# Kernel tuning notes

Measured on AMD Instinct MI355X. Metric: run time of the kernel, lower is better.

The kernel has to match this reference:

```python
import jax, jax.numpy as jnp
import numpy as np

K = 128   # per-head dim == input dim
H = 8     # heads
B = 2
T = 2048


def setup_inputs() -> dict:
    key = jax.random.key(0)
    ks = jax.random.split(key, 6)
    s_in = 1.0 / np.sqrt(K)
    s_out = 1.0 / np.sqrt(K * H)
    return {
        "x": jax.random.normal(ks[0], (B, T, K), dtype=jnp.float32),
        # Linear weights stored as (in, out); torch Linear init ~ U(-1/sqrt(in), 1/sqrt(in))
        "Wq": jax.random.uniform(ks[1], (K, K * H), jnp.float32, -s_in, s_in),
        "Wk": jax.random.uniform(ks[2], (K, K * H), jnp.float32, -s_in, s_in),
        "Wv": jax.random.uniform(ks[3], (K, K * H), jnp.float32, -s_in, s_in),
        "Wo": jax.random.uniform(ks[4], (K * H, K), jnp.float32, -s_out, s_out),
        "bo": jax.random.uniform(ks[5], (K,), jnp.float32, -s_out, s_out),
    }


def reference(x, Wq, Wk, Wv, Wo, bo):
    b, t, k = x.shape
    h = H
    scale = k ** 0.25
    # projections -> [b, t, h, k]
    q = (x @ Wq).reshape(b, t, h, k) / scale
    ke = (x @ Wk).reshape(b, t, h, k) / scale
    v = (x @ Wv).reshape(b, t, h, k)
    # scores: [b, h, t, t]
    scores = jnp.einsum('bihk,bjhk->bhij', q, ke)
    # causal mask: positions j > i get -inf (diagonal kept)
    causal = jnp.tril(jnp.ones((t, t), dtype=bool))
    scores = jnp.where(causal[None, None], scores, -jnp.inf)
    p = jax.nn.softmax(scores, axis=-1)
    out = jnp.einsum('bhij,bjhk->bihk', p, v).reshape(b, t, h * k)
    return out @ Wo + bo
```

## Files before the change

### kernel.cpp

```cpp
#include <hip/hip_runtime.h>

typedef __bf16 bf16;
typedef __bf16 bf16x4 __attribute__((ext_vector_type(4)));
typedef __bf16 bf16x8 __attribute__((ext_vector_type(8)));
typedef float f32x4 __attribute__((ext_vector_type(4)));
typedef float f32x16 __attribute__((ext_vector_type(16)));
typedef int i32x4 __attribute__((ext_vector_type(4)));

#define MFMA16(a, b, c) __builtin_amdgcn_mfma_f32_16x16x32_bf16((a), (b), (c), 0, 0, 0)
#define MFMA32(a, b, c) __builtin_amdgcn_mfma_f32_32x32x16_bf16((a), (b), (c), 0, 0, 0)

__device__ __forceinline__ int swz16(int r, int c) { return (c ^ (r & 15)); }

__device__ __forceinline__ int cvt_pk_bf16(float lo, float hi) {
  int r;
  asm("v_cvt_pk_bf16_f32 %0, %1, %2" : "=v"(r) : "v"(lo), "v"(hi));
  return r;
}

__global__ __launch_bounds__(256) void trW_kernel(
    const float* __restrict__ Wq, const float* __restrict__ Wk,
    const float* __restrict__ Wv, const float* __restrict__ Wo,
    bf16* __restrict__ outbase) {
  __shared__ bf16 tile[32][33];
  const int z = blockIdx.z;
  const float* ib = (z == 0) ? Wq : (z == 1) ? Wk : (z == 2) ? Wv : Wo;
  bf16* ob = outbase + (size_t)z * 131072;
  const int R = (z < 3) ? 128 : 1024;
  const int C = (z < 3) ? 1024 : 128;
  int r0 = (z < 3) ? blockIdx.y * 32 : blockIdx.x * 32;
  int c0 = (z < 3) ? blockIdx.x * 32 : blockIdx.y * 32;
  int tx = threadIdx.x & 31, ty = threadIdx.x >> 5;
#pragma unroll
  for (int i = 0; i < 4; ++i) {
    int r = ty + i * 8;
    tile[r][tx] = (bf16)ib[(size_t)(r0 + r) * C + (c0 + tx)];
  }
  __syncthreads();
#pragma unroll
  for (int i = 0; i < 4; ++i) {
    int r = ty + i * 8;
    ob[(size_t)(c0 + r) * R + (r0 + tx)] = tile[tx][r];
  }
}

__global__ __launch_bounds__(256) void proj_gemm(
    const float* __restrict__ x, const bf16* __restrict__ Wqt,
    const bf16* __restrict__ Wkt, const bf16* __restrict__ Wvt,
    bf16* __restrict__ Qf, bf16* __restrict__ Kf, bf16* __restrict__ Vf) {
  __shared__ __align__(16) bf16 As[128 * 128];
  __shared__ __align__(16) bf16 Bs[128 * 128];
  const int mt = blockIdx.x;
  const int nt = blockIdx.y;
  const int matid = nt >> 3, h = nt & 7;
  const bf16* W = (matid == 0) ? Wqt : (matid == 1) ? Wkt : Wvt;
  const int tid = threadIdx.x;
  const bf16* sb = W + (size_t)h * 128 * 128;
#pragma unroll
  for (int i = 0; i < 8; ++i) {
    int c = tid + i * 256;
    int r = c >> 4, cc = c & 15;
    const f32x4* p = (const f32x4*)(x + (size_t)(mt * 128 + r) * 128 + cc * 8);
    f32x4 a = p[0], b = p[1];
    bf16x8 o;
#pragma unroll
    for (int j = 0; j < 4; ++j) { o[j] = (bf16)a[j]; o[4 + j] = (bf16)b[j]; }
    *(bf16x8*)&As[r * 128 + swz16(r, cc) * 8] = o;
  }
#pragma unroll
  for (int i = 0; i < 8; ++i) {
    int c = tid + i * 256;
    int r = c >> 4, cc = c & 15;
    *(bf16x8*)&Bs[r * 128 + swz16(r, cc) * 8] = *(const bf16x8*)(sb + (size_t)r * 128 + cc * 8);
  }
  __syncthreads();
  const int wave = tid >> 6, lane = tid & 63;
  const int wr = (wave >> 1) * 64, wc = (wave & 1) * 64;
  const int lr = lane & 15, lkb = lane >> 4;
  const f32x4 FZ = {0.f, 0.f, 0.f, 0.f};
  f32x4 acc[4][4];
#pragma unroll
  for (int mf = 0; mf < 4; ++mf)
#pragma unroll
    for (int nf = 0; nf < 4; ++nf) acc[mf][nf] = FZ;
  const bool qk = (matid < 2);
#pragma unroll
  for (int ks = 0; ks < 4; ++ks) {
    bf16x8 a[4], b[4];
#pragma unroll
    for (int mf = 0; mf < 4; ++mf) {
      int r = wr + mf * 16 + lr;
      a[mf] = *(const bf16x8*)&As[r * 128 + swz16(r, ks * 4 + lkb) * 8];
    }
#pragma unroll
    for (int nf = 0; nf < 4; ++nf) {
      int r = wc + nf * 16 + lr;
      b[nf] = *(const bf16x8*)&Bs[r * 128 + swz16(r, ks * 4 + lkb) * 8];
    }
    if (qk) {
#pragma unroll
      for (int mf = 0; mf < 4; ++mf)
#pragma unroll
        for (int nf = 0; nf < 4; ++nf) acc[mf][nf] = MFMA16(b[nf], a[mf], acc[mf][nf]);
    } else {
#pragma unroll
      for (int mf = 0; mf < 4; ++mf)
#pragma unroll
        for (int nf = 0; nf < 4; ++nf) acc[mf][nf] = MFMA16(a[mf], b[nf], acc[mf][nf]);
    }
  }
  const int rb = lkb * 4;
  if (qk) {
    bf16* Out = (matid == 0) ? Qf : Kf;
#pragma unroll
    for (int mf = 0; mf < 4; ++mf)
#pragma unroll
      for (int nf = 0; nf < 4; ++nf) {
        int m = mt * 128 + wr + mf * 16 + lr;
        int d0 = wc + nf * 16 + rb;
        int bb = m >> 11, t = m & 2047;
        bf16x4 vv;
#pragma unroll
        for (int r = 0; r < 4; ++r) vv[r] = (bf16)acc[mf][nf][r];
        size_t e = (size_t)(bb * 8 + h) * 262144
                 + (size_t)(((t >> 5) * 8 + (d0 >> 4)) * 512 + ((d0 >> 3) & 1) * 256
                            + (t & 31) * 8 + (d0 & 7));
        *(bf16x4*)(Out + e) = vv;
      }
  } else {
#pragma unroll
    for (int mf = 0; mf < 4; ++mf)
#pragma unroll
      for (int nf = 0; nf < 4; ++nf) {
        int d = wc + nf * 16 + lr;
        int m0 = mt * 128 + wr + mf * 16 + rb;
        int bb = m0 >> 11, t0 = m0 & 2047;
        bf16x4 vv;
#pragma unroll
        for (int r = 0; r < 4; ++r) vv[r] = (bf16)acc[mf][nf][r];
        size_t e = (size_t)(bb * 8 + h) * 262144
                 + (size_t)((d >> 5) * 65536 + (t0 >> 4) * 512 + ((t0 >> 3) & 1) * 256
                            + (d & 31) * 8 + (t0 & 7));
        *(bf16x4*)(Vf + e) = vv;
      }
  }
}

__global__ __launch_bounds__(128) void attn_kernel(
    bf16* __restrict__ Qf, const bf16* __restrict__ Kf, const bf16* __restrict__ Vf) {
  __shared__ float Om[128 * 32];
  __shared__ float Lm[32];
  __shared__ float Ll[32];
  const int bid = blockIdx.x;
  const int bh = (bid & 7) | (((bid >> 3) & 1) << 3);
  const int j = bid >> 4;
  const int v = j & 15, m4 = j >> 4;
  const int qt = (m4 == 0) ? v : (m4 == 1) ? 31 - v : (m4 == 2) ? 32 + v : 63 - v;
  const int nT = (qt >> 1) + 1;
  const int h0 = (nT + 1) >> 1, h1 = nT - h0;
  const int tid = threadIdx.x;
  const int g = tid >> 6, lane = tid & 63;
  const int lq = lane & 31, hi = lane >> 5;
  const int q0 = qt * 32;
  const int hg = g ? h1 : h0;
  const int tb = g ? h0 : 0;
  const bf16* Qh = Qf + (size_t)bh * 262144;
  const bf16* Kh = Kf + (size_t)bh * 262144;
  const bf16* Vh = Vf + (size_t)bh * 262144;
  const float SCL = 0.12751744f;
  const int lo = hi * 256 + lq * 8;

  bf16x8 qf[8];
#pragma unroll
  for (int ks = 0; ks < 8; ++ks)
    qf[ks] = *(const bf16x8*)(Qh + qt * 4096 + ks * 512 + lo);

  float mrun = -__builtin_inff(), lrun = 0.f;
  f32x16 O[4];
#pragma unroll
  for (int dt = 0; dt < 4; ++dt)
#pragma unroll
    for (int r = 0; r < 16; ++r) O[dt][r] = 0.f;

  for (int it = 0; it < hg; ++it) {
    const int kvt = tb + it;
    const int kv0 = kvt * 64;
    const bf16* kbase = Kh + kvt * 8192 + lo;
    bf16x8 ka[8], kb[8];
#pragma unroll
    for (int i = 0; i < 8; ++i) ka[i] = *(const bf16x8*)(kbase + i * 512);
#pragma unroll
    for (int i = 0; i < 8; ++i) kb[i] = *(const bf16x8*)(kbase + 4096 + i * 512);
    f32x16 p0, p1;
#pragma unroll
    for (int r = 0; r < 16; ++r) { p0[r] = 0.f; p1[r] = 0.f; }
#pragma unroll
    for (int ks = 0; ks < 8; ++ks) p0 = MFMA32(ka[ks], qf[ks], p0);
#pragma unroll
    for (int ks = 0; ks < 8; ++ks) p1 = MFMA32(kb[ks], qf[ks], p1);
    if (kvt == (qt >> 1)) {
      const int qg = q0 + lq;
#pragma unroll
      for (int r = 0; r < 16; ++r) {
        int kvr = kv0 + (r & 3) + 8 * (r >> 2) + 4 * hi;
        if (kvr > qg) p0[r] = -__builtin_inff();
        if (kvr + 32 > qg) p1[r] = -__builtin_inff();
      }
    }
    float pm = -__builtin_inff();
#pragma unroll
    for (int r = 0; r < 16; ++r) pm = fmaxf(pm, fmaxf(p0[r], p1[r]));
    pm = fmaxf(pm, __shfl_xor(pm, 32, 64));
    float pmS = pm * SCL;
    if (!__all(pmS <= mrun + 8.f)) {
      float mnew = fmaxf(mrun, pmS);
      float alpha = exp2f(mrun - mnew);
      mrun = mnew;
      lrun *= alpha;
#pragma unroll
      for (int dt = 0; dt < 4; ++dt)
#pragma unroll
        for (int r = 0; r < 16; ++r) O[dt][r] *= alpha;
    }
    float ps = 0.f;
#pragma unroll
    for (int r = 0; r < 16; ++r) {
      float a = exp2f(__builtin_fmaf(p0[r], SCL, -mrun));
      float b = exp2f(__builtin_fmaf(p1[r], SCL, -mrun));
      p0[r] = a; p1[r] = b;
      ps += a + b;
    }
    ps += __shfl_xor(ps, 32, 64);
    lrun += ps;
    int w[16];
#pragma unroll
    for (int i = 0; i < 8; ++i) w[i] = cvt_pk_bf16(p0[2 * i], p0[2 * i + 1]);
#pragma unroll
    for (int i = 0; i < 8; ++i) w[8 + i] = cvt_pk_bf16(p1[2 * i], p1[2 * i + 1]);
    bf16x8 pa[4];
#pragma unroll
    for (int t4 = 0; t4 < 4; ++t4) {
      int b0 = t4 * 4;
      int e0 = __shfl_xor(w[b0 + 0], 32, 64);
      int e1 = __shfl_xor(w[b0 + 1], 32, 64);
      int e2 = __shfl_xor(w[b0 + 2], 32, 64);
      int e3 = __shfl_xor(w[b0 + 3], 32, 64);
      i32x4 f;
      f[0] = hi ? e2 : w[b0 + 0];
      f[1] = hi ? e3 : w[b0 + 1];
      f[2] = hi ? w[b0 + 2] : e0;
      f[3] = hi ? w[b0 + 3] : e1;
      pa[t4] = __builtin_bit_cast(bf16x8, f);
    }
    const bf16* vbase = Vh + (kvt * 4) * 512 + lo;
#pragma unroll
    for (int dt = 0; dt < 4; ++dt) {
      bf16x8 va0 = *(const bf16x8*)(vbase + dt * 65536 + 0 * 512);
      bf16x8 va1 = *(const bf16x8*)(vbase + dt * 65536 + 1 * 512);
      bf16x8 va2 = *(const bf16x8*)(vbase + dt * 65536 + 2 * 512);
      bf16x8 va3 = *(const bf16x8*)(vbase + dt * 65536 + 3 * 512);
      O[dt] = MFMA32(va0, pa[0], O[dt]);
      O[dt] = MFMA32(va1, pa[1], O[dt]);
      O[dt] = MFMA32(va2, pa[2], O[dt]);
      O[dt] = MFMA32(va3, pa[3], O[dt]);
    }
  }

  if (g == 1) {
#pragma unroll
    for (int dt = 0; dt < 4; ++dt)
#pragma unroll
      for (int r = 0; r < 16; ++r)
        Om[(dt * 32 + (r & 3) + 8 * (r >> 2) + 4 * hi) * 32 + lq] = O[dt][r];
    if (!hi) { Lm[lq] = mrun; Ll[lq] = lrun; }
  }
  __syncthreads();
  if (g == 0) {
    float m1 = Lm[lq], l1 = Ll[lq];
    float mF = fmaxf(mrun, m1);
    float a0 = exp2f(mrun - mF), a1 = exp2f(m1 - mF);
    float inv = 1.f / (lrun * a0 + l1 * a1);
    bf16* qw = Qf + (size_t)bh * 262144 + qt * 4096 + lq * 8 + 4 * hi;
#pragma unroll
    for (int dt = 0; dt < 4; ++dt) {
#pragma unroll
      for (int rq = 0; rq < 4; ++rq) {
        bf16x4 vv;
#pragma unroll
        for (int jj = 0; jj < 4; ++jj) {
          int r = rq * 4 + jj;
          int d = dt * 32 + jj + 8 * rq + 4 * hi;
          float o1 = Om[d * 32 + lq];
          vv[jj] = (bf16)((O[dt][r] * a0 + o1 * a1) * inv);
        }
        *(bf16x4*)(qw + (dt * 2 + (rq >> 1)) * 512 + (rq & 1) * 256) = vv;
      }
    }
  }
}

__global__ __launch_bounds__(256) void outproj_kernel(
    const bf16* __restrict__ AO, const bf16* __restrict__ Wot,
    const float* __restrict__ bo, float* __restrict__ out) {
  __shared__ __align__(16) bf16 As[16 * 128];
  __shared__ __align__(16) bf16 Bs[128 * 128];
  const f32x4 FZ = {0.f, 0.f, 0.f, 0.f};
  const int mt = blockIdx.x;
  const int tid = threadIdx.x, wave = tid >> 6, lane = tid & 63;
  const int lr = lane & 15, lkb = lane >> 4, rb = lkb * 4;
  const int wc = wave * 32;
  f32x4 acc[2];
  acc[0] = FZ; acc[1] = FZ;
  for (int kt = 0; kt < 8; ++kt) {
    __syncthreads();
    {
      int r = tid >> 4, cc = tid & 15;
      int m = mt * 16 + r, bb = m >> 11, t = m & 2047;
      const bf16* src = AO + (size_t)(bb * 8 + kt) * 262144
          + ((t >> 5) * 8 + (cc >> 1)) * 512 + (cc & 1) * 256 + (t & 31) * 8;
      *(bf16x8*)&As[r * 128 + swz16(r, cc) * 8] = *(const bf16x8*)src;
    }
#pragma unroll
    for (int i = 0; i < 8; ++i) {
      int c = tid + i * 256;
      int r = c >> 4, cc = c & 15;
      *(bf16x8*)&Bs[r * 128 + swz16(r, cc) * 8] =
          *(const bf16x8*)(Wot + (size_t)r * 1024 + kt * 128 + cc * 8);
    }
    __syncthreads();
#pragma unroll
    for (int ks = 0; ks < 4; ++ks) {
      bf16x8 a = *(const bf16x8*)&As[lr * 128 + swz16(lr, ks * 4 + lkb) * 8];
#pragma unroll
      for (int nf = 0; nf < 2; ++nf) {
        int r = wc + nf * 16 + lr;
        bf16x8 b = *(const bf16x8*)&Bs[r * 128 + swz16(r, ks * 4 + lkb) * 8];
        acc[nf] = MFMA16(a, b, acc[nf]);
      }
    }
  }
#pragma unroll
  for (int nf = 0; nf < 2; ++nf)
#pragma unroll
    for (int r = 0; r < 4; ++r) {
      int m = mt * 16 + rb + r;
      int n = wc + nf * 16 + lr;
      out[(size_t)m * 128 + n] = acc[nf][r] + bo[n];
    }
}

extern "C" void kernel_launch(void* const* d_in, const int* in_sizes, int n_in,
                              void* d_out, int out_size, void* d_ws, size_t ws_size,
                              hipStream_t stream) {
  (void)in_sizes; (void)n_in; (void)out_size; (void)ws_size;
  const float* x  = (const float*)d_in[0];
  const float* Wq = (const float*)d_in[1];
  const float* Wk = (const float*)d_in[2];
  const float* Wv = (const float*)d_in[3];
  const float* Wo = (const float*)d_in[4];
  const float* bo = (const float*)d_in[5];
  float* out = (float*)d_out;

  bf16* ws  = (bf16*)d_ws;
  bf16* Wqt = ws;
  bf16* Wkt = Wqt + 131072;
  bf16* Wvt = Wkt + 131072;
  bf16* Wot = Wvt + 131072;
  bf16* Qf  = Wot + 131072;
  bf16* Kf  = Qf + 4194304;
  bf16* Vf  = Kf + 4194304;

  trW_kernel<<<dim3(32, 4, 4), 256, 0, stream>>>(Wq, Wk, Wv, Wo, Wqt);
  proj_gemm<<<dim3(32, 24, 1), 256, 0, stream>>>(x, Wqt, Wkt, Wvt, Qf, Kf, Vf);
  attn_kernel<<<dim3(1024, 1, 1), 128, 0, stream>>>(Qf, Kf, Vf);
  outproj_kernel<<<dim3(256, 1, 1), 256, 0, stream>>>(Qf, Wot, bo, out);
}
```

Measured before the change: 146.5 us.

## Split causal KV range across four waves and pair query tiles per block

The attention kernel now runs 256 threads per block, and each block handles two complementary query tiles (pr and 63-pr) in sequence so causal work is balanced across blocks. The KV range of each tile is split across four waves, with the split direction reversed in the second phase, and the partial results are merged through a two-level shared-memory reduction with extra barriers. The change also prefetches V fragments before the softmax, raises wave priority around the MFMA sections, and splits the max and sum reductions into four independent chains for more ILP. The cost is more register pressure from holding V in registers, more LDS use, and more synchronization, in exchange for halving the grid and getting more even per-block work.

```diff
diff --git a/kernel.cpp b/kernel.cpp
--- a/kernel.cpp
+++ b/kernel.cpp
@@ -146,156 +146,199 @@
   }
 }
 
-__global__ __launch_bounds__(128) void attn_kernel(
+__global__ __launch_bounds__(256) void attn_kernel(
     bf16* __restrict__ Qf, const bf16* __restrict__ Kf, const bf16* __restrict__ Vf) {
-  __shared__ float Om[128 * 32];
-  __shared__ float Lm[32];
-  __shared__ float Ll[32];
+  __shared__ float Om0[128 * 32];
+  __shared__ float Om1[128 * 32];
+  __shared__ float L0m[32], L0l[32], L1m[32], L1l[32];
   const int bid = blockIdx.x;
-  const int bh = (bid & 7) | (((bid >> 3) & 1) << 3);
-  const int j = bid >> 4;
-  const int v = j & 15, m4 = j >> 4;
-  const int qt = (m4 == 0) ? v : (m4 == 1) ? 31 - v : (m4 == 2) ? 32 + v : 63 - v;
-  const int nT = (qt >> 1) + 1;
-  const int h0 = (nT + 1) >> 1, h1 = nT - h0;
+  const int bh = bid & 15;
+  const int pr = bid >> 4;
   const int tid = threadIdx.x;
-  const int g = tid >> 6, lane = tid & 63;
+  const int w = tid >> 6, lane = tid & 63;
   const int lq = lane & 31, hi = lane >> 5;
-  const int q0 = qt * 32;
-  const int hg = g ? h1 : h0;
-  const int tb = g ? h0 : 0;
+  const int lo = hi * 256 + lq * 8;
   const bf16* Qh = Qf + (size_t)bh * 262144;
   const bf16* Kh = Kf + (size_t)bh * 262144;
   const bf16* Vh = Vf + (size_t)bh * 262144;
   const float SCL = 0.12751744f;
-  const int lo = hi * 256 + lq * 8;
-
-  bf16x8 qf[8];
-#pragma unroll
-  for (int ks = 0; ks < 8; ++ks)
-    qf[ks] = *(const bf16x8*)(Qh + qt * 4096 + ks * 512 + lo);
-
-  float mrun = -__builtin_inff(), lrun = 0.f;
-  f32x16 O[4];
-#pragma unroll
-  for (int dt = 0; dt < 4; ++dt)
-#pragma unroll
-    for (int r = 0; r < 16; ++r) O[dt][r] = 0.f;
-
-  for (int it = 0; it < hg; ++it) {
-    const int kvt = tb + it;
-    const int kv0 = kvt * 64;
-    const bf16* kbase = Kh + kvt * 8192 + lo;
-    bf16x8 ka[8], kb[8];
-#pragma unroll
-    for (int i = 0; i < 8; ++i) ka[i] = *(const bf16x8*)(kbase + i * 512);
-#pragma unroll
-    for (int i = 0; i < 8; ++i) kb[i] = *(const bf16x8*)(kbase + 4096 + i * 512);
-    f32x16 p0, p1;
-#pragma unroll
-    for (int r = 0; r < 16; ++r) { p0[r] = 0.f; p1[r] = 0.f; }
-#pragma unroll
-    for (int ks = 0; ks < 8; ++ks) p0 = MFMA32(ka[ks], qf[ks], p0);
-#pragma unroll
-    for (int ks = 0; ks < 8; ++ks) p1 = MFMA32(kb[ks], qf[ks], p1);
-    if (kvt == (qt >> 1)) {
-      const int qg = q0 + lq;
-#pragma unroll
-      for (int r = 0; r < 16; ++r) {
-        int kvr = kv0 + (r & 3) + 8 * (r >> 2) + 4 * hi;
-        if (kvr > qg) p0[r] = -__builtin_inff();
-        if (kvr + 32 > qg) p1[r] = -__builtin_inff();
-      }
-    }
-    float pm = -__builtin_inff();
-#pragma unroll
-    for (int r = 0; r < 16; ++r) pm = fmaxf(pm, fmaxf(p0[r], p1[r]));
-    pm = fmaxf(pm, __shfl_xor(pm, 32, 64));
-    float pmS = pm * SCL;
-    if (!__all(pmS <= mrun + 8.f)) {
-      float mnew = fmaxf(mrun, pmS);
-      float alpha = exp2f(mrun - mnew);
-      mrun = mnew;
-      lrun *= alpha;
+
+  for (int ph = 0; ph < 2; ++ph) {
+    const int qt = ph ? (63 - pr) : pr;
+    const int nT = (qt >> 1) + 1;
+    const int base = nT >> 2, rem = nT & 3;
+    const int we = ph ? (3 - w) : w;
+    const int cnt = base + (we < rem ? 1 : 0);
+    const int tb = we * base + (we < rem ? we : rem);
+
+    bf16x8 qf[8];
+#pragma unroll
+    for (int ks = 0; ks < 8; ++ks)
+      qf[ks] = *(const bf16x8*)(Qh + qt * 4096 + ks * 512 + lo);
+
+    float mrun = -__builtin_inff(), lrun = 0.f;
+    f32x16 O[4];
+#pragma unroll
+    for (int dt = 0; dt < 4; ++dt)
+#pragma unroll
+      for (int r = 0; r < 16; ++r) O[dt][r] = 0.f;
+
+    for (int it = 0; it < cnt; ++it) {
+      const int kvt = tb + it;
+      const int kv0 = kvt * 64;
+      const bf16* kbase = Kh + kvt * 8192 + lo;
+      bf16x8 ka[8], kb[8];
+#pragma unroll
+      for (int i = 0; i < 8; ++i) ka[i] = *(const bf16x8*)(kbase + i * 512);
+#pragma unroll
+      for (int i = 0; i < 8; ++i) kb[i] = *(const bf16x8*)(kbase + 4096 + i * 512);
+      f32x16 p0, p1;
+#pragma unroll
+      for (int r = 0; r < 16; ++r) { p0[r] = 0.f; p1[r] = 0.f; }
+      __builtin_amdgcn_s_setprio(1);
+#pragma unroll
+      for (int ks = 0; ks < 8; ++ks) p0 = MFMA32(ka[ks], qf[ks], p0);
+#pragma unroll
+      for (int ks = 0; ks < 8; ++ks) p1 = MFMA32(kb[ks], qf[ks], p1);
+      __builtin_amdgcn_s_setprio(0);
+      const bf16* vbase = Vh + kvt * 2048 + lo;
+      bf16x8 va[16];
+#pragma unroll
+      for (int i = 0; i < 16; ++i)
+        va[i] = *(const bf16x8*)(vbase + (i >> 2) * 65536 + (i & 3) * 512);
+      if (kvt == (qt >> 1)) {
+        const int qg = qt * 32 + lq;
+#pragma unroll
+        for (int r = 0; r < 16; ++r) {
+          int kvr = kv0 + (r & 3) + 8 * (r >> 2) + 4 * hi;
+          if (kvr > qg) p0[r] = -__builtin_inff();
+          if (kvr + 32 > qg) p1[r] = -__builtin_inff();
+        }
+      }
+      float m0 = fmaxf(p0[0], p1[0]);
+      float m1_ = fmaxf(p0[1], p1[1]);
+      float m2 = fmaxf(p0[2], p1[2]);
+      float m3 = fmaxf(p0[3], p1[3]);
+#pragma unroll
+      for (int r = 4; r < 16; r += 4) {
+        m0 = fmaxf(m0, fmaxf(p0[r], p1[r]));
+        m1_ = fmaxf(m1_, fmaxf(p0[r + 1], p1[r + 1]));
+        m2 = fmaxf(m2, fmaxf(p0[r + 2], p1[r + 2]));
+        m3 = fmaxf(m3, fmaxf(p0[r + 3], p1[r + 3]));
+      }
+      float pm = fmaxf(fmaxf(m0, m1_), fmaxf(m2, m3));
+      pm = fmaxf(pm, __shfl_xor(pm, 32, 64));
+      float pmS = pm * SCL;
+      if (!__all(pmS <= mrun + 8.f)) {
+        float mnew = fmaxf(mrun, pmS);
+        float alpha = exp2f(mrun - mnew);
+        mrun = mnew;
+        lrun *= alpha;
+#pragma unroll
+        for (int dt = 0; dt < 4; ++dt)
+#pragma unroll
+          for (int r = 0; r < 16; ++r) O[dt][r] *= alpha;
+      }
+      float s0 = 0.f, s1 = 0.f, s2 = 0.f, s3 = 0.f;
+#pragma unroll
+      for (int r = 0; r < 16; r += 4) {
+        float a0_ = exp2f(__builtin_fmaf(p0[r], SCL, -mrun));
+        float a1_ = exp2f(__builtin_fmaf(p0[r + 1], SCL, -mrun));
+        float a2_ = exp2f(__builtin_fmaf(p0[r + 2], SCL, -mrun));
+        float a3_ = exp2f(__builtin_fmaf(p0[r + 3], SCL, -mrun));
+        float b0_ = exp2f(__builtin_fmaf(p1[r], SCL, -mrun));
+        float b1_ = exp2f(__builtin_fmaf(p1[r + 1], SCL, -mrun));
+        float b2_ = exp2f(__builtin_fmaf(p1[r + 2], SCL, -mrun));
+        float b3_ = exp2f(__builtin_fmaf(p1[r + 3], SCL, -mrun));
+        p0[r] = a0_; p0[r + 1] = a1_; p0[r + 2] = a2_; p0[r + 3] = a3_;
+        p1[r] = b0_; p1[r + 1] = b1_; p1[r + 2] = b2_; p1[r + 3] = b3_;
+        s0 += a0_ + b0_; s1 += a1_ + b1_; s2 += a2_ + b2_; s3 += a3_ + b3_;
+      }
+      float ps = (s0 + s1) + (s2 + s3);
+      ps += __shfl_xor(ps, 32, 64);
+      lrun += ps;
+      int wd[16];
+#pragma unroll
+      for (int i = 0; i < 8; ++i) wd[i] = cvt_pk_bf16(p0[2 * i], p0[2 * i + 1]);
+#pragma unroll
+      for (int i = 0; i < 8; ++i) wd[8 + i] = cvt_pk_bf16(p1[2 * i], p1[2 * i + 1]);
+      bf16x8 pa[4];
+#pragma unroll
+      for (int t4 = 0; t4 < 4; ++t4) {
+        int b0 = t4 * 4;
+        int e0 = __shfl_xor(wd[b0 + 0], 32, 64);
+        int e1 = __shfl_xor(wd[b0 + 1], 32, 64);
+        int e2 = __shfl_xor(wd[b0 + 2], 32, 64);
+        int e3 = __shfl_xor(wd[b0 + 3], 32, 64);
+        i32x4 f;
+        f[0] = hi ? e2 : wd[b0 + 0];
+        f[1] = hi ? e3 : wd[b0 + 1];
+        f[2] = hi ? wd[b0 + 2] : e0;
+        f[3] = hi ? wd[b0 + 3] : e1;
+        pa[t4] = __builtin_bit_cast(bf16x8, f);
+      }
+      __builtin_amdgcn_s_setprio(1);
+#pragma unroll
+      for (int dt = 0; dt < 4; ++dt) {
+        O[dt] = MFMA32(va[dt * 4 + 0], pa[0], O[dt]);
+        O[dt] = MFMA32(va[dt * 4 + 1], pa[1], O[dt]);
+        O[dt] = MFMA32(va[dt * 4 + 2], pa[2], O[dt]);
+        O[dt] = MFMA32(va[dt * 4 + 3], pa[3], O[dt]);
+      }
+      __builtin_amdgcn_s_setprio(0);
+    }
+
+    auto STORE = [&](float* Om, float* Lm, float* Ll) {
 #pragma unroll
       for (int dt = 0; dt < 4; ++dt)
 #pragma unroll
-        for (int r = 0; r < 16; ++r) O[dt][r] *= alpha;
-    }
-    float ps = 0.f;
-#pragma unroll
-    for (int r = 0; r < 16; ++r) {
-      float a = exp2f(__builtin_fmaf(p0[r], SCL, -mrun));
-      float b = exp2f(__builtin_fmaf(p1[r], SCL, -mrun));
-      p0[r] = a; p1[r] = b;
-      ps += a + b;
-    }
-    ps += __shfl_xor(ps, 32, 64);
-    lrun += ps;
-    int w[16];
-#pragma unroll
-    for (int i = 0; i < 8; ++i) w[i] = cvt_pk_bf16(p0[2 * i], p0[2 * i + 1]);
-#pragma unroll
-    for (int i = 0; i < 8; ++i) w[8 + i] = cvt_pk_bf16(p1[2 * i], p1[2 * i + 1]);
-    bf16x8 pa[4];
-#pragma unroll
-    for (int t4 = 0; t4 < 4; ++t4) {
-      int b0 = t4 * 4;
-      int e0 = __shfl_xor(w[b0 + 0], 32, 64);
-      int e1 = __shfl_xor(w[b0 + 1], 32, 64);
-      int e2 = __shfl_xor(w[b0 + 2], 32, 64);
-      int e3 = __shfl_xor(w[b0 + 3], 32, 64);
-      i32x4 f;
-      f[0] = hi ? e2 : w[b0 + 0];
-      f[1] = hi ? e3 : w[b0 + 1];
-      f[2] = hi ? w[b0 + 2] : e0;
-      f[3] = hi ? w[b0 + 3] : e1;
-      pa[t4] = __builtin_bit_cast(bf16x8, f);
-    }
-    const bf16* vbase = Vh + (kvt * 4) * 512 + lo;
-#pragma unroll
-    for (int dt = 0; dt < 4; ++dt) {
-      bf16x8 va0 = *(const bf16x8*)(vbase + dt * 65536 + 0 * 512);
-      bf16x8 va1 = *(const bf16x8*)(vbase + dt * 65536 + 1 * 512);
-      bf16x8 va2 = *(const bf16x8*)(vbase + dt * 65536 + 2 * 512);
-      bf16x8 va3 = *(const bf16x8*)(vbase + dt * 65536 + 3 * 512);
-      O[dt] = MFMA32(va0, pa[0], O[dt]);
-      O[dt] = MFMA32(va1, pa[1], O[dt]);
-      O[dt] = MFMA32(va2, pa[2], O[dt]);
-      O[dt] = MFMA32(va3, pa[3], O[dt]);
-    }
-  }
-
-  if (g == 1) {
-#pragma unroll
-    for (int dt = 0; dt < 4; ++dt)
-#pragma unroll
-      for (int r = 0; r < 16; ++r)
-        Om[(dt * 32 + (r & 3) + 8 * (r >> 2) + 4 * hi) * 32 + lq] = O[dt][r];
-    if (!hi) { Lm[lq] = mrun; Ll[lq] = lrun; }
-  }
-  __syncthreads();
-  if (g == 0) {
-    float m1 = Lm[lq], l1 = Ll[lq];
-    float mF = fmaxf(mrun, m1);
-    float a0 = exp2f(mrun - mF), a1 = exp2f(m1 - mF);
-    float inv = 1.f / (lrun * a0 + l1 * a1);
-    bf16* qw = Qf + (size_t)bh * 262144 + qt * 4096 + lq * 8 + 4 * hi;
-#pragma unroll
-    for (int dt = 0; dt < 4; ++dt) {
-#pragma unroll
-      for (int rq = 0; rq < 4; ++rq) {
-        bf16x4 vv;
-#pragma unroll
-        for (int jj = 0; jj < 4; ++jj) {
-          int r = rq * 4 + jj;
-          int d = dt * 32 + jj + 8 * rq + 4 * hi;
-          float o1 = Om[d * 32 + lq];
-          vv[jj] = (bf16)((O[dt][r] * a0 + o1 * a1) * inv);
+        for (int r = 0; r < 16; ++r)
+          Om[(dt * 32 + (r & 3) + 8 * (r >> 2) + 4 * hi) * 32 + lq] = O[dt][r];
+      if (!hi) { Lm[lq] = mrun; Ll[lq] = lrun; }
+    };
+    auto MERGE = [&](const float* Om, const float* Lm, const float* Ll) {
+      float m1 = Lm[lq], l1 = Ll[lq];
+      float mF = fmaxf(mrun, m1);
+      float a0 = (mrun < -3.0e38f) ? 0.f : exp2f(mrun - mF);
+      float a1 = (m1 < -3.0e38f) ? 0.f : exp2f(m1 - mF);
+      lrun = lrun * a0 + l1 * a1;
+#pragma unroll
+      for (int dt = 0; dt < 4; ++dt)
+#pragma unroll
+        for (int r = 0; r < 16; ++r)
+          O[dt][r] = O[dt][r] * a0 +
+                     Om[(dt * 32 + (r & 3) + 8 * (r >> 2) + 4 * hi) * 32 + lq] * a1;
+      mrun = mF;
+    };
+
+    __syncthreads();
+    if (w == 1) STORE(Om0, L0m, L0l);
+    if (w == 3) STORE(Om1, L1m, L1l);
+    __syncthreads();
+    if (w == 0) MERGE(Om0, L0m, L0l);
+    if (w == 2) MERGE(Om1, L1m, L1l);
+    __syncthreads();
+    if (w == 2) STORE(Om0, L0m, L0l);
+    __syncthreads();
+    if (w == 0) {
+      MERGE(Om0, L0m, L0l);
+      float inv = 1.f / lrun;
+      bf16* qw = Qf + (size_t)bh * 262144 + qt * 4096 + lq * 8 + 4 * hi;
+#pragma unroll
+      for (int dt = 0; dt < 4; ++dt) {
+#pragma unroll
+        for (int rq = 0; rq < 4; ++rq) {
+          bf16x4 vv;
+#pragma unroll
+          for (int jj = 0; jj < 4; ++jj) {
+            int r = rq * 4 + jj;
+            vv[jj] = (bf16)(O[dt][r] * inv);
+          }
+          *(bf16x4*)(qw + (dt * 2 + (rq >> 1)) * 512 + (rq & 1) * 256) = vv;
         }
-        *(bf16x4*)(qw + (dt * 2 + (rq >> 1)) * 512 + (rq & 1) * 256) = vv;
-      }
-    }
+      }
+    }
+    __syncthreads();
   }
 }
 
@@ -372,6 +415,6 @@
 
   trW_kernel<<<dim3(32, 4, 4), 256, 0, stream>>>(Wq, Wk, Wv, Wo, Wqt);
   proj_gemm<<<dim3(32, 24, 1), 256, 0, stream>>>(x, Wqt, Wkt, Wvt, Qf, Kf, Vf);
-  attn_kernel<<<dim3(1024, 1, 1), 128, 0, stream>>>(Qf, Kf, Vf);
+  attn_kernel<<<dim3(512, 1, 1), 256, 0, stream>>>(Qf, Kf, Vf);
   outproj_kernel<<<dim3(256, 1, 1), 256, 0, stream>>>(Qf, Wot, bo, out);
 }
```

Result: faster. 136.2 us (-7.0%).
